# Optimization experiments

Hardware: AMD Instinct MI355X
Metric: run time of the kernel (lower is better)

Reference implementation:

```python
import jax, jax.numpy as jnp
import numpy as np

DISP = 8 // 2  # self.disp = disp // 2


def setup_inputs() -> dict:
    key = jax.random.key(0)
    inputs = jax.random.normal(key, (1, 16, 9, 256, 256), dtype=jnp.float32)
    return {"inputs": inputs}


def reference(inputs) -> jnp.ndarray:
    # inputs: [b, c, A, h, w]
    b, c, A, h, w = inputs.shape
    ds = jnp.arange(-DISP, DISP + 1)            # [D] disparity hypotheses
    a_off = jnp.arange(A) - A // 2              # [A] angular offsets
    t = ds[:, None] * a_off[None, :]            # [D, A] shift per (d, a)

    # roll by t with zero-fill == gather from index (i - t), masked to in-range
    hi = jnp.arange(h)[None, None, :] - t[:, :, None]   # [D, A, h]
    wi = jnp.arange(w)[None, None, :] - t[:, :, None]   # [D, A, w]
    h_valid = (hi >= 0) & (hi < h)
    w_valid = (wi >= 0) & (wi < w)
    hi = jnp.clip(hi, 0, h - 1)
    wi = jnp.clip(wi, 0, w - 1)

    # broadcast index arrays to [D, A, h, w]
    a_idx = jnp.arange(A)[None, :, None, None]
    h_idx = hi[:, :, :, None]
    w_idx = wi[:, :, None, :]
    gathered = inputs[:, :, a_idx, h_idx, w_idx]        # [b, c, D, A, h, w]

    mask = (h_valid[:, :, :, None] & w_valid[:, :, None, :])  # [D, A, h, w]
    out = gathered * mask.astype(inputs.dtype)

    # torch.stack(..., dim=1) -> [b, D, c, A, h, w]
    return jnp.transpose(out, (0, 2, 1, 3, 4, 5))
```

## Files before the change

kernel.cpp:

```cpp
#include <hip/hip_runtime.h>


#define RTILE 16
#define MAXROWS 48

__global__ __launch_bounds__(256) void cost_volume_kernel(
    const float* __restrict__ in, float* __restrict__ out)
{
    __shared__ float lds[MAXROWS * 256];

    int ca = blockIdx.y;
    int c = ca / 9;
    int a = ca - c * 9;
    int y0 = blockIdx.x * RTILE;

    int tx = threadIdx.x;
    int ty = threadIdx.y;

    int a4 = a - 4;
    int H = 4 * (a4 < 0 ? -a4 : a4);
    int nrows = RTILE + 2 * H;
    int base = y0 - H;

    const float* __restrict__ slice = in + ((long)ca * 256) * 256;
    for (int r0 = 0; r0 < nrows; r0 += 4) {
        int r = r0 + ty;
        if (r < nrows) {
            int g = base + r;
            float4 v = make_float4(0.f, 0.f, 0.f, 0.f);
            if (g >= 0 && g < 256)
                v = *reinterpret_cast<const float4*>(slice + g * 256 + tx * 4);
            *reinterpret_cast<float4*>(&lds[r * 256 + tx * 4]) = v;
        }
    }
    __syncthreads();

    #pragma unroll
    for (int d = 0; d < 9; ++d) {
        int t = (d - 4) * a4;
        long obase = (((long)(d * 16 + c) * 9 + a) * 256L);
        for (int yb = ty; yb < RTILE; yb += 4) {
            int y = y0 + yb;
            int lr = y - t - base;
            const float* __restrict__ lrow = &lds[lr * 256];
            float* __restrict__ orow = out + (obase + y) * 256L;
            #pragma unroll
            for (int e = 0; e < 4; ++e) {
                int x = tx + 64 * e;
                int xx = x - t;
                float v = (xx >= 0 && xx < 256) ? lrow[xx] : 0.f;
                __builtin_nontemporal_store(v, orow + x);
            }
        }
    }
}

extern "C" void kernel_launch(void* const* d_in, const int* in_sizes, int n_in,
                              void* d_out, int out_size, void* d_ws, size_t ws_size,
                              hipStream_t stream)
{
    const float* in = (const float*)d_in[0];
    float* out = (float*)d_out;

    dim3 block(64, 4, 1);
    dim3 grid(16, 144, 1);
    cost_volume_kernel<<<grid, block, 0, stream>>>(in, out);
}
```

Measured before the change: 71.94 us.

## Scatter from input-row tiles instead of gathering shifted halo rows

Each block now loads only its own 16 input rows into LDS and scatters them to the shifted output rows for every disparity, instead of loading a halo of up to 48 rows per block. Edge blocks additionally write the zero-filled rows that no input row maps to. This removes redundant global reads and shrinks LDS use, which may raise occupancy. In exchange, output writes per block land on non-contiguous rows, and correctness depends on the zero-fill rows exactly covering the uncovered range.

```diff
diff --git a/kernel.cpp b/kernel.cpp
--- a/kernel.cpp
+++ b/kernel.cpp
@@ -2,48 +2,40 @@
 
 
 #define RTILE 16
-#define MAXROWS 48
 
 __global__ __launch_bounds__(256) void cost_volume_kernel(
     const float* __restrict__ in, float* __restrict__ out)
 {
-    __shared__ float lds[MAXROWS * 256];
+    __shared__ float lds[RTILE * 256];
 
     int ca = blockIdx.y;
     int c = ca / 9;
     int a = ca - c * 9;
-    int y0 = blockIdx.x * RTILE;
+    int a4 = a - 4;
+    int g0 = blockIdx.x * RTILE;
 
     int tx = threadIdx.x;
     int ty = threadIdx.y;
 
-    int a4 = a - 4;
-    int H = 4 * (a4 < 0 ? -a4 : a4);
-    int nrows = RTILE + 2 * H;
-    int base = y0 - H;
-
-    const float* __restrict__ slice = in + ((long)ca * 256) * 256;
-    for (int r0 = 0; r0 < nrows; r0 += 4) {
+    const float* __restrict__ slice = in + (long)ca * 256 * 256;
+    #pragma unroll
+    for (int r0 = 0; r0 < RTILE; r0 += 4) {
         int r = r0 + ty;
-        if (r < nrows) {
-            int g = base + r;
-            float4 v = make_float4(0.f, 0.f, 0.f, 0.f);
-            if (g >= 0 && g < 256)
-                v = *reinterpret_cast<const float4*>(slice + g * 256 + tx * 4);
-            *reinterpret_cast<float4*>(&lds[r * 256 + tx * 4]) = v;
-        }
+        *reinterpret_cast<float4*>(&lds[r * 256 + tx * 4]) =
+            *reinterpret_cast<const float4*>(slice + (long)(g0 + r) * 256 + tx * 4);
     }
     __syncthreads();
 
     #pragma unroll
     for (int d = 0; d < 9; ++d) {
         int t = (d - 4) * a4;
-        long obase = (((long)(d * 16 + c) * 9 + a) * 256L);
+        float* __restrict__ oplane = out + ((long)(d * 16 + c) * 9 + a) * 256L * 256L;
+
         for (int yb = ty; yb < RTILE; yb += 4) {
-            int y = y0 + yb;
-            int lr = y - t - base;
-            const float* __restrict__ lrow = &lds[lr * 256];
-            float* __restrict__ orow = out + (obase + y) * 256L;
+            int y = g0 + yb + t;
+            if (y < 0 || y >= 256) continue;
+            const float* __restrict__ lrow = &lds[yb * 256];
+            float* __restrict__ orow = oplane + (long)y * 256;
             #pragma unroll
             for (int e = 0; e < 4; ++e) {
                 int x = tx + 64 * e;
@@ -51,6 +43,16 @@
                 float v = (xx >= 0 && xx < 256) ? lrow[xx] : 0.f;
                 __builtin_nontemporal_store(v, orow + x);
             }
+        }
+
+        int z0 = 0, zn = 0;
+        if (t > 0 && g0 == 0)                { z0 = 0;       zn = t;  }
+        else if (t < 0 && g0 == 256 - RTILE) { z0 = 256 + t; zn = -t; }
+        for (int yb = ty; yb < zn; yb += 4) {
+            float* __restrict__ orow = oplane + (long)(z0 + yb) * 256;
+            #pragma unroll
+            for (int e = 0; e < 4; ++e)
+                __builtin_nontemporal_store(0.f, orow + tx + 64 * e);
         }
     }
 }
```

Result: no change. 70.57 us (-1.9%).
